# Optimization experiments

Hardware: AMD Instinct MI355X
Metric: run time of the kernel (lower is better)

Reference implementation:

```python
import jax, jax.numpy as jnp
import numpy as np

MAX_ITER = 10
EPS = 1e-4


def setup_inputs() -> dict:
    key = jax.random.key(0)
    k1, k2, k3 = jax.random.split(key, 3)
    B, N, M = 64, 1024, 1024
    s = jax.random.uniform(k1, (B, N, M), dtype=jnp.float32)
    nrows = jax.random.randint(k2, (B,), 0, N, dtype=jnp.int64 if jax.config.read('jax_enable_x64') else jnp.int32)
    ncols = jax.random.randint(k3, (B,), 0, M, dtype=nrows.dtype)
    return {"s": s, "nrows": nrows, "ncols": ncols}


def _sinkhorn(s, nrows, ncols):
    # Faithful to torch Sinkhorn.forward with exp=False, dummy_row=False.
    # The torch code builds [B,N,N]/[B,M,M] block-of-ones matrices and matmuls;
    # mathematically this is a masked column-sum (even iters) / row-sum (odd iters)
    # over the valid nrows[b] x ncols[b] block, followed by division inside the
    # block and zeroing outside it.
    B, N, M = s.shape
    row_mask = jnp.arange(N)[None, :] < nrows[:, None]            # [B, N]
    col_mask = jnp.arange(M)[None, :] < ncols[:, None]            # [B, M]
    mask = row_mask[:, :, None] & col_mask[:, None, :]            # [B, N, M]

    out = s + EPS
    for i in range(MAX_ITER):
        if i % 2 == 0:
            # column sums over valid rows -> [B, 1, M]
            sm = jnp.sum(jnp.where(row_mask[:, :, None], out, 0.0), axis=1, keepdims=True)
        else:
            # row sums over valid cols -> [B, N, 1]
            sm = jnp.sum(jnp.where(col_mask[:, None, :], out, 0.0), axis=2, keepdims=True)
        sm = jnp.where(sm == 0, 1.0, sm)  # guard (only affects masked-out entries)
        out = jnp.where(mask, out / sm, 0.0)
    return out


def reference(s, nrows, ncols):
    return _sinkhorn(s, nrows, ncols)
```

## Files before the change

kernel.cpp:

```cpp
#include <hip/hip_runtime.h>
#include <hip/hip_fp16.h>

#define EPS 1e-4f
constexpr int N_DIM = 1024;
constexpr int M_DIM = 1024;
constexpr int BATCH = 64;
constexpr int CH    = 16;
constexpr int CROWS = N_DIM / CH;



__global__ __launch_bounds__(256)
void col_first_conv(const float* __restrict__ s,
                    const int* __restrict__ nrows,
                    const int* __restrict__ ncols,
                    __half* __restrict__ h,
                    float* __restrict__ tpart) {
    const int b  = blockIdx.y;
    const int mt = blockIdx.x & 3;
    const int ch = blockIdx.x >> 2;
    const int R = nrows[b], C = ncols[b];
    const int lane = threadIdx.x & 63, wv = threadIdx.x >> 6;
    const int m = mt * 256 + lane * 4;
    const int n0 = ch * CROWS;
    const int nend = min(R, n0 + CROWS);
    const size_t base = (size_t)b * N_DIM * M_DIM;

    float4 acc = make_float4(0.f, 0.f, 0.f, 0.f);
    if (mt * 256 < C) {
        for (int n = n0 + wv; n < nend; n += 4) {
            float4 v = *(const float4*)(s + base + (size_t)n * M_DIM + m);
            v.x = (m + 0 < C) ? v.x + EPS : 0.f;
            v.y = (m + 1 < C) ? v.y + EPS : 0.f;
            v.z = (m + 2 < C) ? v.z + EPS : 0.f;
            v.w = (m + 3 < C) ? v.w + EPS : 0.f;
            acc.x += v.x; acc.y += v.y; acc.z += v.z; acc.w += v.w;
            union { __half2 h2[2]; uint2 u2; } pk;
            pk.h2[0] = __floats2half2_rn(v.x, v.y);
            pk.h2[1] = __floats2half2_rn(v.z, v.w);
            *(uint2*)(h + base + (size_t)n * M_DIM + m) = pk.u2;
        }
    } else {
        const uint2 z = make_uint2(0u, 0u);
        for (int n = n0 + wv; n < nend; n += 4)
            *(uint2*)(h + base + (size_t)n * M_DIM + m) = z;
    }
    __shared__ float4 red[4][64];
    red[wv][lane] = acc;
    __syncthreads();
    if (wv == 0) {
        float4 a0 = red[0][lane], a1 = red[1][lane],
               a2 = red[2][lane], a3 = red[3][lane];
        float4 t = make_float4(a0.x + a1.x + a2.x + a3.x,
                               a0.y + a1.y + a2.y + a3.y,
                               a0.z + a1.z + a2.z + a3.z,
                               a0.w + a1.w + a2.w + a3.w);
        *(float4*)(tpart + (size_t)(ch * BATCH + b) * M_DIM + m) = t;
    }
}

__global__ __launch_bounds__(256)
void col_h(const __half* __restrict__ h,
           const int* __restrict__ nrows,
           const int* __restrict__ ncols,
           const float* __restrict__ u,
           float* __restrict__ tpart) {
    const int b  = blockIdx.y;
    const int mt = blockIdx.x & 1;
    const int ch = blockIdx.x >> 1;
    const int R = nrows[b], C = ncols[b];
    const int lane = threadIdx.x & 63, wv = threadIdx.x >> 6;
    const int m = mt * 512 + lane * 8;
    const int n0 = ch * CROWS;
    const int nend = min(R, n0 + CROWS);
    const size_t base = (size_t)b * N_DIM * M_DIM;

    __shared__ float rlds[CROWS];
    if (threadIdx.x < CROWS) {
        float uu = u[b * N_DIM + n0 + threadIdx.x];
        rlds[threadIdx.x] = (uu == 0.f) ? 1.f : 1.f / uu;
    }
    __syncthreads();

    float acc[8] = {0.f, 0.f, 0.f, 0.f, 0.f, 0.f, 0.f, 0.f};
    if (mt * 512 < C) {
        for (int n = n0 + wv; n < nend; n += 4) {
            uint4 raw = *(const uint4*)(h + base + (size_t)n * M_DIM + m);
            const float rn = rlds[n - n0];
            const __half2* hp = (const __half2*)&raw;
#pragma unroll
            for (int k = 0; k < 4; ++k) {
                float2 f = __half22float2(hp[k]);
                acc[2 * k]     += rn * f.x;
                acc[2 * k + 1] += rn * f.y;
            }
        }
    }
    __shared__ float red[4][64 * 8];
#pragma unroll
    for (int k = 0; k < 8; ++k) red[wv][lane * 8 + k] = acc[k];
    __syncthreads();
    if (wv == 0) {
        float t[8];
#pragma unroll
        for (int k = 0; k < 8; ++k)
            t[k] = red[0][lane * 8 + k] + red[1][lane * 8 + k] +
                   red[2][lane * 8 + k] + red[3][lane * 8 + k];
        float* tp = tpart + (size_t)(ch * BATCH + b) * M_DIM + m;
        *(float4*)tp       = make_float4(t[0], t[1], t[2], t[3]);
        *(float4*)(tp + 4) = make_float4(t[4], t[5], t[6], t[7]);
    }
}

template <bool WRITE_C>
__global__ __launch_bounds__(256)
void row_h(const __half* __restrict__ h,
           const int* __restrict__ nrows,
           const int* __restrict__ ncols,
           const float* __restrict__ tpart,
           float* __restrict__ u,
           float* __restrict__ cOut) {
    const int b = blockIdx.y;
    const int R = nrows[b], C = ncols[b];
    const int n0 = blockIdx.x * 32;
    if (n0 >= R) return;
    const size_t base = (size_t)b * N_DIM * M_DIM;

    __shared__ float clds[M_DIM];
    {
        const int t4 = threadIdx.x * 4;
        float4 sum = make_float4(0.f, 0.f, 0.f, 0.f);
#pragma unroll
        for (int ch = 0; ch < CH; ++ch) {
            float4 p = *(const float4*)(tpart + (size_t)(ch * BATCH + b) * M_DIM + t4);
            sum.x += p.x; sum.y += p.y; sum.z += p.z; sum.w += p.w;
        }
        float4 cv;
        cv.x = (sum.x == 0.f) ? 1.f : 1.f / sum.x;
        cv.y = (sum.y == 0.f) ? 1.f : 1.f / sum.y;
        cv.z = (sum.z == 0.f) ? 1.f : 1.f / sum.z;
        cv.w = (sum.w == 0.f) ? 1.f : 1.f / sum.w;
        *(float4*)&clds[t4] = cv;
        if (WRITE_C && blockIdx.x == 0)
            *(float4*)(cOut + b * M_DIM + t4) = cv;
    }
    __syncthreads();

    const int lane = threadIdx.x & 63, wv = threadIdx.x >> 6;
    const bool hi = (C > 512);
#pragma unroll 2
    for (int i = 0; i < 8; ++i) {
        const int n = n0 + wv * 8 + i;
        if (n >= R) break;
        const __half* hrow = h + base + (size_t)n * M_DIM;
        float sum = 0.f;
        {
            uint4 raw = *(const uint4*)(hrow + lane * 8);
            const __half2* hp = (const __half2*)&raw;
            const float* cl = &clds[lane * 8];
#pragma unroll
            for (int k = 0; k < 4; ++k) {
                float2 f = __half22float2(hp[k]);
                sum += f.x * cl[2 * k] + f.y * cl[2 * k + 1];
            }
        }
        if (hi) {
            uint4 raw = *(const uint4*)(hrow + 512 + lane * 8);
            const __half2* hp = (const __half2*)&raw;
            const float* cl = &clds[512 + lane * 8];
#pragma unroll
            for (int k = 0; k < 4; ++k) {
                float2 f = __half22float2(hp[k]);
                sum += f.x * cl[2 * k] + f.y * cl[2 * k + 1];
            }
        }
#pragma unroll
        for (int off = 32; off; off >>= 1) sum += __shfl_down(sum, off);
        if (lane == 0) u[b * N_DIM + n] = sum;
    }
}

__global__ __launch_bounds__(256)
void finalize(const float* __restrict__ s,
              const int* __restrict__ nrows,
              const int* __restrict__ ncols,
              const float* __restrict__ u,
              const float* __restrict__ c,
              float* __restrict__ out) {
    const int n = blockIdx.x;
    const int b = blockIdx.y;
    const int R = nrows[b], C = ncols[b];
    const size_t base = ((size_t)b * N_DIM + n) * M_DIM;
    const int m = threadIdx.x * 4;

    float4 o = make_float4(0.f, 0.f, 0.f, 0.f);
    if (n < R && m < C) {
        float uu = u[b * N_DIM + n];
        float rn = (uu == 0.f) ? 1.f : 1.f / uu;
        float4 v  = *(const float4*)(s + base + m);
        float4 cc = *(const float4*)(c + b * M_DIM + m);
        o.x = (m + 0 < C) ? (v.x + EPS) * rn * cc.x : 0.f;
        o.y = (m + 1 < C) ? (v.y + EPS) * rn * cc.y : 0.f;
        o.z = (m + 2 < C) ? (v.z + EPS) * rn * cc.z : 0.f;
        o.w = (m + 3 < C) ? (v.w + EPS) * rn * cc.w : 0.f;
    }
    *(float4*)(out + base + m) = o;
}

template <bool FIRST, int CHUNKS>
__global__ __launch_bounds__(256)
void col_sweep(const float* __restrict__ s, const int* __restrict__ nrows,
               const int* __restrict__ ncols, const float* __restrict__ u,
               float* __restrict__ tpart) {
    const int b  = blockIdx.y;
    const int mt = blockIdx.x & 3;
    const int ch = blockIdx.x >> 2;
    const int R = nrows[b], C = ncols[b];
    const int lane = threadIdx.x & 63, wv = threadIdx.x >> 6;
    const int m0 = mt * 256;
    const int m  = m0 + lane * 4;
    constexpr int RW = N_DIM / CHUNKS;
    const int n0 = ch * RW;
    const int nend = min(R, n0 + RW);

    __shared__ float rlds[RW > 1024 ? 1 : RW];
    if (!FIRST) {
        for (int i = threadIdx.x; i < RW; i += 256) {
            float uu = u[b * N_DIM + n0 + i];
            rlds[i] = (uu == 0.f) ? 1.f : 1.f / uu;
        }
        __syncthreads();
    }
    float4 acc = make_float4(0.f, 0.f, 0.f, 0.f);
    if (m0 < C) {
        const float* __restrict__ sb = s + (size_t)b * N_DIM * M_DIM;
#pragma unroll 4
        for (int n = n0 + wv; n < nend; n += 4) {
            float4 v = *(const float4*)(sb + (size_t)n * M_DIM + m);
            float rn = FIRST ? 1.f : rlds[n - n0];
            acc.x += rn * (v.x + EPS); acc.y += rn * (v.y + EPS);
            acc.z += rn * (v.z + EPS); acc.w += rn * (v.w + EPS);
        }
    }
    __shared__ float4 red[4][64];
    red[wv][lane] = acc;
    __syncthreads();
    if (wv == 0) {
        float4 a0 = red[0][lane], a1 = red[1][lane],
               a2 = red[2][lane], a3 = red[3][lane];
        float4 t = make_float4(a0.x + a1.x + a2.x + a3.x, a0.y + a1.y + a2.y + a3.y,
                               a0.z + a1.z + a2.z + a3.z, a0.w + a1.w + a2.w + a3.w);
        *(float4*)(tpart + ((size_t)(ch * BATCH + b)) * M_DIM + m) = t;
    }
}

template <int CHUNKS, bool WRITE_C>
__global__ __launch_bounds__(256)
void row_sweep(const float* __restrict__ s, const int* __restrict__ nrows,
               const int* __restrict__ ncols, const float* __restrict__ tpart,
               float* __restrict__ u, float* __restrict__ cOut) {
    const int b = blockIdx.y;
    const int R = nrows[b], C = ncols[b];
    const int n0 = blockIdx.x * 16;
    if (n0 >= R) return;
    __shared__ float clds[M_DIM];
    {
        const int t4 = threadIdx.x;
        float4 sum = make_float4(0.f, 0.f, 0.f, 0.f);
#pragma unroll
        for (int ch = 0; ch < CHUNKS; ++ch) {
            float4 p = *(const float4*)(tpart + ((size_t)(ch * BATCH + b)) * M_DIM + t4 * 4);
            sum.x += p.x; sum.y += p.y; sum.z += p.z; sum.w += p.w;
        }
        float4 cv;
        cv.x = (sum.x == 0.f) ? 1.f : 1.f / sum.x;
        cv.y = (sum.y == 0.f) ? 1.f : 1.f / sum.y;
        cv.z = (sum.z == 0.f) ? 1.f : 1.f / sum.z;
        cv.w = (sum.w == 0.f) ? 1.f : 1.f / sum.w;
        *(float4*)&clds[t4 * 4] = cv;
        if (WRITE_C && blockIdx.x == 0)
            *(float4*)(cOut + b * M_DIM + t4 * 4) = cv;
    }
    __syncthreads();
    const int lane = threadIdx.x & 63, wv = threadIdx.x >> 6;
    const int C4 = C >> 2;
#pragma unroll
    for (int i = 0; i < 4; ++i) {
        const int n = n0 + wv * 4 + i;
        if (n >= R) break;
        const float* __restrict__ srow = s + ((size_t)b * N_DIM + n) * M_DIM;
        float sum = 0.f;
        for (int j = lane; j < C4; j += 64) {
            float4 v  = ((const float4*)srow)[j];
            float4 cc = *(const float4*)&clds[j * 4];
            sum += (v.x + EPS) * cc.x + (v.y + EPS) * cc.y +
                   (v.z + EPS) * cc.z + (v.w + EPS) * cc.w;
        }
        for (int mm = (C4 << 2) + lane; mm < C; mm += 64)
            sum += (srow[mm] + EPS) * clds[mm];
#pragma unroll
        for (int off = 32; off; off >>= 1) sum += __shfl_down(sum, off);
        if (lane == 0) u[b * N_DIM + n] = sum;
    }
}

extern "C" void kernel_launch(void* const* d_in, const int* in_sizes, int n_in,
                              void* d_out, int out_size, void* d_ws, size_t ws_size,
                              hipStream_t stream) {
    const float* s     = (const float*)d_in[0];
    const int*   nrows = (const int*)d_in[1];
    const int*   ncols = (const int*)d_in[2];
    float*       out   = (float*)d_out;

    const size_t hElems   = (size_t)BATCH * N_DIM * M_DIM;
    const size_t need_f16 = hElems * 2 +
                            ((size_t)CH * BATCH * M_DIM + BATCH * N_DIM + BATCH * M_DIM) * 4;

    if (ws_size >= need_f16) {
        __half* h     = (__half*)d_ws;
        float*  tpart = (float*)(h + hElems);
        float*  u     = tpart + (size_t)CH * BATCH * M_DIM;
        float*  c     = u + (size_t)BATCH * N_DIM;

        dim3 colGrid1(4 * CH, BATCH);
        dim3 colGridH(2 * CH, BATCH);
        dim3 rowGridH(32, BATCH);

        col_first_conv<<<colGrid1, 256, 0, stream>>>(s, nrows, ncols, h, tpart);
        row_h<false><<<rowGridH, 256, 0, stream>>>(h, nrows, ncols, tpart, u, c);
        for (int k = 0; k < 3; ++k) {
            col_h<<<colGridH, 256, 0, stream>>>(h, nrows, ncols, u, tpart);
            row_h<false><<<rowGridH, 256, 0, stream>>>(h, nrows, ncols, tpart, u, c);
        }
        col_h<<<colGridH, 256, 0, stream>>>(h, nrows, ncols, u, tpart);
        row_h<true><<<rowGridH, 256, 0, stream>>>(h, nrows, ncols, tpart, u, c);
        finalize<<<dim3(N_DIM, BATCH), 256, 0, stream>>>(s, nrows, ncols, u, c, out);
        return;
    }

    const size_t need4 = (size_t)(4 * BATCH * M_DIM + BATCH * N_DIM + BATCH * M_DIM) * 4;
    if (ws_size >= need4) {
        float* tpart = (float*)d_ws;
        float* u = tpart + (size_t)4 * BATCH * M_DIM;
        float* c = u + (size_t)BATCH * N_DIM;
        dim3 colGrid(16, BATCH), rowGrid(64, BATCH);
        col_sweep<true, 4><<<colGrid, 256, 0, stream>>>(s, nrows, ncols, u, tpart);
        row_sweep<4, false><<<rowGrid, 256, 0, stream>>>(s, nrows, ncols, tpart, u, c);
        for (int k = 1; k < 4; ++k) {
            col_sweep<false, 4><<<colGrid, 256, 0, stream>>>(s, nrows, ncols, u, tpart);
            row_sweep<4, false><<<rowGrid, 256, 0, stream>>>(s, nrows, ncols, tpart, u, c);
        }
        col_sweep<false, 4><<<colGrid, 256, 0, stream>>>(s, nrows, ncols, u, tpart);
        row_sweep<4, true><<<rowGrid, 256, 0, stream>>>(s, nrows, ncols, tpart, u, c);
        finalize<<<dim3(N_DIM, BATCH), 256, 0, stream>>>(s, nrows, ncols, u, c, out);
    } else {
        float* tpart = (float*)d_ws;
        float* u = tpart + (size_t)BATCH * M_DIM;
        float* c = u + (size_t)BATCH * N_DIM;
        dim3 colGrid(4, BATCH), rowGrid(64, BATCH);
        col_sweep<true, 1><<<colGrid, 256, 0, stream>>>(s, nrows, ncols, u, tpart);
        row_sweep<1, false><<<rowGrid, 256, 0, stream>>>(s, nrows, ncols, tpart, u, c);
        for (int k = 1; k < 4; ++k) {
            col_sweep<false, 1><<<colGrid, 256, 0, stream>>>(s, nrows, ncols, u, tpart);
            row_sweep<1, false><<<rowGrid, 256, 0, stream>>>(s, nrows, ncols, tpart, u, c);
        }
        col_sweep<false, 1><<<colGrid, 256, 0, stream>>>(s, nrows, ncols, u, tpart);
        row_sweep<1, true><<<rowGrid, 256, 0, stream>>>(s, nrows, ncols, tpart, u, c);
        finalize<<<dim3(N_DIM, BATCH), 256, 0, stream>>>(s, nrows, ncols, u, c, out);
    }
}
```

Baseline: 239.0 us.

## Fuse final row normalization with output write and halve column chunks

Replaces the last row_h plus finalize pass with a single row_final kernel that computes row sums from the fp16 copy, then immediately writes the normalized output from registers, avoiding a re-read of the fp32 input. Also reduces column-partial chunks from 16 to 8, fewer tpart partials to reduce at the cost of longer per-block row loops. The output is now derived from the fp16 copy rather than the original fp32 s, which may reduce accuracy.

```diff
diff --git a/kernel.cpp b/kernel.cpp
--- a/kernel.cpp
+++ b/kernel.cpp
@@ -5,7 +5,7 @@
 constexpr int N_DIM = 1024;
 constexpr int M_DIM = 1024;
 constexpr int BATCH = 64;
-constexpr int CH    = 16;
+constexpr int CH    = 8;
 constexpr int CROWS = N_DIM / CH;
 
 
@@ -76,9 +76,9 @@
     const size_t base = (size_t)b * N_DIM * M_DIM;
 
     __shared__ float rlds[CROWS];
-    if (threadIdx.x < CROWS) {
-        float uu = u[b * N_DIM + n0 + threadIdx.x];
-        rlds[threadIdx.x] = (uu == 0.f) ? 1.f : 1.f / uu;
+    for (int i = threadIdx.x; i < CROWS; i += 256) {
+        float uu = u[b * N_DIM + n0 + i];
+        rlds[i] = (uu == 0.f) ? 1.f : 1.f / uu;
     }
     __syncthreads();
 
@@ -112,14 +112,12 @@
     }
 }
 
-template <bool WRITE_C>
 __global__ __launch_bounds__(256)
 void row_h(const __half* __restrict__ h,
            const int* __restrict__ nrows,
            const int* __restrict__ ncols,
            const float* __restrict__ tpart,
-           float* __restrict__ u,
-           float* __restrict__ cOut) {
+           float* __restrict__ u) {
     const int b = blockIdx.y;
     const int R = nrows[b], C = ncols[b];
     const int n0 = blockIdx.x * 32;
@@ -141,8 +139,6 @@
         cv.z = (sum.z == 0.f) ? 1.f : 1.f / sum.z;
         cv.w = (sum.w == 0.f) ? 1.f : 1.f / sum.w;
         *(float4*)&clds[t4] = cv;
-        if (WRITE_C && blockIdx.x == 0)
-            *(float4*)(cOut + b * M_DIM + t4) = cv;
     }
     __syncthreads();
 
@@ -181,12 +177,194 @@
 }
 
 __global__ __launch_bounds__(256)
-void finalize(const float* __restrict__ s,
-              const int* __restrict__ nrows,
-              const int* __restrict__ ncols,
-              const float* __restrict__ u,
-              const float* __restrict__ c,
-              float* __restrict__ out) {
+void row_final(const __half* __restrict__ h,
+               const int* __restrict__ nrows,
+               const int* __restrict__ ncols,
+               const float* __restrict__ tpart,
+               float* __restrict__ out) {
+    const int b = blockIdx.y;
+    const int R = nrows[b], C = ncols[b];
+    const int n0 = blockIdx.x * 32;
+    const size_t base = (size_t)b * N_DIM * M_DIM;
+
+    __shared__ float clds[M_DIM];
+    {
+        const int t4 = threadIdx.x * 4;
+        float4 sum = make_float4(0.f, 0.f, 0.f, 0.f);
+#pragma unroll
+        for (int ch = 0; ch < CH; ++ch) {
+            float4 p = *(const float4*)(tpart + (size_t)(ch * BATCH + b) * M_DIM + t4);
+            sum.x += p.x; sum.y += p.y; sum.z += p.z; sum.w += p.w;
+        }
+        float4 cv;
+        cv.x = (sum.x == 0.f) ? 1.f : 1.f / sum.x;
+        cv.y = (sum.y == 0.f) ? 1.f : 1.f / sum.y;
+        cv.z = (sum.z == 0.f) ? 1.f : 1.f / sum.z;
+        cv.w = (sum.w == 0.f) ? 1.f : 1.f / sum.w;
+        *(float4*)&clds[t4] = cv;
+    }
+    __syncthreads();
+
+    const int lane = threadIdx.x & 63, wv = threadIdx.x >> 6;
+    const bool hi = (C > 512);
+    const float4 z4 = make_float4(0.f, 0.f, 0.f, 0.f);
+
+    for (int i = 0; i < 8; ++i) {
+        const int n = n0 + wv * 8 + i;
+        float* orow = out + base + (size_t)n * M_DIM;
+        float4 o0 = z4, o1 = z4, o2 = z4, o3 = z4;
+        if (n < R) {
+            const __half* hrow = h + base + (size_t)n * M_DIM;
+            uint4 rlo = *(const uint4*)(hrow + lane * 8);
+            uint4 rhi;
+            float flo[8], fhi[8];
+            const __half2* hp = (const __half2*)&rlo;
+#pragma unroll
+            for (int k = 0; k < 4; ++k) {
+                float2 f = __half22float2(hp[k]);
+                flo[2 * k] = f.x; flo[2 * k + 1] = f.y;
+            }
+            const float* cl = &clds[lane * 8];
+            float sum = 0.f;
+#pragma unroll
+            for (int k = 0; k < 8; ++k) sum += flo[k] * cl[k];
+            if (hi) {
+                rhi = *(const uint4*)(hrow + 512 + lane * 8);
+                const __half2* hq = (const __half2*)&rhi;
+#pragma unroll
+                for (int k = 0; k < 4; ++k) {
+                    float2 f = __half22float2(hq[k]);
+                    fhi[2 * k] = f.x; fhi[2 * k + 1] = f.y;
+                }
+                const float* ch2 = &clds[512 + lane * 8];
+#pragma unroll
+                for (int k = 0; k < 8; ++k) sum += fhi[k] * ch2[k];
+            }
+#pragma unroll
+            for (int off = 32; off; off >>= 1) sum += __shfl_down(sum, off);
+            float tot = __shfl(sum, 0);
+            const float rn = (tot == 0.f) ? 1.f : 1.f / tot;
+
+            o0 = make_float4(flo[0] * rn * cl[0], flo[1] * rn * cl[1],
+                             flo[2] * rn * cl[2], flo[3] * rn * cl[3]);
+            o1 = make_float4(flo[4] * rn * cl[4], flo[5] * rn * cl[5],
+                             flo[6] * rn * cl[6], flo[7] * rn * cl[7]);
+            if (hi) {
+                const float* ch2 = &clds[512 + lane * 8];
+                o2 = make_float4(fhi[0] * rn * ch2[0], fhi[1] * rn * ch2[1],
+                                 fhi[2] * rn * ch2[2], fhi[3] * rn * ch2[3]);
+                o3 = make_float4(fhi[4] * rn * ch2[4], fhi[5] * rn * ch2[5],
+                                 fhi[6] * rn * ch2[6], fhi[7] * rn * ch2[7]);
+            }
+        }
+        *(float4*)(orow + lane * 8)           = o0;
+        *(float4*)(orow + lane * 8 + 4)       = o1;
+        *(float4*)(orow + 512 + lane * 8)     = o2;
+        *(float4*)(orow + 512 + lane * 8 + 4) = o3;
+    }
+}
+
+template <bool FIRST, int CHUNKS>
+__global__ __launch_bounds__(256)
+void col_sweep(const float* __restrict__ s, const int* __restrict__ nrows,
+               const int* __restrict__ ncols, const float* __restrict__ u,
+               float* __restrict__ tpart) {
+    const int b  = blockIdx.y;
+    const int mt = blockIdx.x & 3;
+    const int ch = blockIdx.x >> 2;
+    const int R = nrows[b], C = ncols[b];
+    const int lane = threadIdx.x & 63, wv = threadIdx.x >> 6;
+    const int m0 = mt * 256;
+    const int m  = m0 + lane * 4;
+    constexpr int RW = N_DIM / CHUNKS;
+    const int n0 = ch * RW;
+    const int nend = min(R, n0 + RW);
+
+    __shared__ float rlds[RW > 1024 ? 1 : RW];
+    if (!FIRST) {
+        for (int i = threadIdx.x; i < RW; i += 256) {
+            float uu = u[b * N_DIM + n0 + i];
+            rlds[i] = (uu == 0.f) ? 1.f : 1.f / uu;
+        }
+        __syncthreads();
+    }
+    float4 acc = make_float4(0.f, 0.f, 0.f, 0.f);
+    if (m0 < C) {
+        const float* __restrict__ sb = s + (size_t)b * N_DIM * M_DIM;
+#pragma unroll 4
+        for (int n = n0 + wv; n < nend; n += 4) {
+            float4 v = *(const float4*)(sb + (size_t)n * M_DIM + m);
+            float rn = FIRST ? 1.f : rlds[n - n0];
+            acc.x += rn * (v.x + EPS); acc.y += rn * (v.y + EPS);
+            acc.z += rn * (v.z + EPS); acc.w += rn * (v.w + EPS);
+        }
+    }
+    __shared__ float4 red[4][64];
+    red[wv][lane] = acc;
+    __syncthreads();
+    if (wv == 0) {
+        float4 a0 = red[0][lane], a1 = red[1][lane],
+               a2 = red[2][lane], a3 = red[3][lane];
+        float4 t = make_float4(a0.x + a1.x + a2.x + a3.x, a0.y + a1.y + a2.y + a3.y,
+                               a0.z + a1.z + a2.z + a3.z, a0.w + a1.w + a2.w + a3.w);
+        *(float4*)(tpart + ((size_t)(ch * BATCH + b)) * M_DIM + m) = t;
+    }
+}
+
+template <int CHUNKS, bool WRITE_C>
+__global__ __launch_bounds__(256)
+void row_sweep(const float* __restrict__ s, const int* __restrict__ nrows,
+               const int* __restrict__ ncols, const float* __restrict__ tpart,
+               float* __restrict__ u, float* __restrict__ cOut) {
+    const int b = blockIdx.y;
+    const int R = nrows[b], C = ncols[b];
+    const int n0 = blockIdx.x * 16;
+    if (n0 >= R) return;
+    __shared__ float clds[M_DIM];
+    {
+        const int t4 = threadIdx.x;
+        float4 sum = make_float4(0.f, 0.f, 0.f, 0.f);
+#pragma unroll
+        for (int ch = 0; ch < CHUNKS; ++ch) {
+            float4 p = *(const float4*)(tpart + ((size_t)(ch * BATCH + b)) * M_DIM + t4 * 4);
+            sum.x += p.x; sum.y += p.y; sum.z += p.z; sum.w += p.w;
+        }
+        float4 cv;
+        cv.x = (sum.x == 0.f) ? 1.f : 1.f / sum.x;
+        cv.y = (sum.y == 0.f) ? 1.f : 1.f / sum.y;
+        cv.z = (sum.z == 0.f) ? 1.f : 1.f / sum.z;
+        cv.w = (sum.w == 0.f) ? 1.f : 1.f / sum.w;
+        *(float4*)&clds[t4 * 4] = cv;
+        if (WRITE_C && blockIdx.x == 0)
+            *(float4*)(cOut + b * M_DIM + t4 * 4) = cv;
+    }
+    __syncthreads();
+    const int lane = threadIdx.x & 63, wv = threadIdx.x >> 6;
+    const int C4 = C >> 2;
+#pragma unroll
+    for (int i = 0; i < 4; ++i) {
+        const int n = n0 + wv * 4 + i;
+        if (n >= R) break;
+        const float* __restrict__ srow = s + ((size_t)b * N_DIM + n) * M_DIM;
+        float sum = 0.f;
+        for (int j = lane; j < C4; j += 64) {
+            float4 v  = ((const float4*)srow)[j];
+            float4 cc = *(const float4*)&clds[j * 4];
+            sum += (v.x + EPS) * cc.x + (v.y + EPS) * cc.y +
+                   (v.z + EPS) * cc.z + (v.w + EPS) * cc.w;
+        }
+        for (int mm = (C4 << 2) + lane; mm < C; mm += 64)
+            sum += (srow[mm] + EPS) * clds[mm];
+#pragma unroll
+        for (int off = 32; off; off >>= 1) sum += __shfl_down(sum, off);
+        if (lane == 0) u[b * N_DIM + n] = sum;
+    }
+}
+
+__global__ __launch_bounds__(256)
+void finalize(const float* __restrict__ s, const int* __restrict__ nrows,
+              const int* __restrict__ ncols, const float* __restrict__ u,
+              const float* __restrict__ c, float* __restrict__ out) {
     const int n = blockIdx.x;
     const int b = blockIdx.y;
     const int R = nrows[b], C = ncols[b];
@@ -207,103 +385,6 @@
     *(float4*)(out + base + m) = o;
 }
 
-template <bool FIRST, int CHUNKS>
-__global__ __launch_bounds__(256)
-void col_sweep(const float* __restrict__ s, const int* __restrict__ nrows,
-               const int* __restrict__ ncols, const float* __restrict__ u,
-               float* __restrict__ tpart) {
-    const int b  = blockIdx.y;
-    const int mt = blockIdx.x & 3;
-    const int ch = blockIdx.x >> 2;
-    const int R = nrows[b], C = ncols[b];
-    const int lane = threadIdx.x & 63, wv = threadIdx.x >> 6;
-    const int m0 = mt * 256;
-    const int m  = m0 + lane * 4;
-    constexpr int RW = N_DIM / CHUNKS;
-    const int n0 = ch * RW;
-    const int nend = min(R, n0 + RW);
-
-    __shared__ float rlds[RW > 1024 ? 1 : RW];
-    if (!FIRST) {
-        for (int i = threadIdx.x; i < RW; i += 256) {
-            float uu = u[b * N_DIM + n0 + i];
-            rlds[i] = (uu == 0.f) ? 1.f : 1.f / uu;
-        }
-        __syncthreads();
-    }
-    float4 acc = make_float4(0.f, 0.f, 0.f, 0.f);
-    if (m0 < C) {
-        const float* __restrict__ sb = s + (size_t)b * N_DIM * M_DIM;
-#pragma unroll 4
-        for (int n = n0 + wv; n < nend; n += 4) {
-            float4 v = *(const float4*)(sb + (size_t)n * M_DIM + m);
-            float rn = FIRST ? 1.f : rlds[n - n0];
-            acc.x += rn * (v.x + EPS); acc.y += rn * (v.y + EPS);
-            acc.z += rn * (v.z + EPS); acc.w += rn * (v.w + EPS);
-        }
-    }
-    __shared__ float4 red[4][64];
-    red[wv][lane] = acc;
-    __syncthreads();
-    if (wv == 0) {
-        float4 a0 = red[0][lane], a1 = red[1][lane],
-               a2 = red[2][lane], a3 = red[3][lane];
-        float4 t = make_float4(a0.x + a1.x + a2.x + a3.x, a0.y + a1.y + a2.y + a3.y,
-                               a0.z + a1.z + a2.z + a3.z, a0.w + a1.w + a2.w + a3.w);
-        *(float4*)(tpart + ((size_t)(ch * BATCH + b)) * M_DIM + m) = t;
-    }
-}
-
-template <int CHUNKS, bool WRITE_C>
-__global__ __launch_bounds__(256)
-void row_sweep(const float* __restrict__ s, const int* __restrict__ nrows,
-               const int* __restrict__ ncols, const float* __restrict__ tpart,
-               float* __restrict__ u, float* __restrict__ cOut) {
-    const int b = blockIdx.y;
-    const int R = nrows[b], C = ncols[b];
-    const int n0 = blockIdx.x * 16;
-    if (n0 >= R) return;
-    __shared__ float clds[M_DIM];
-    {
-        const int t4 = threadIdx.x;
-        float4 sum = make_float4(0.f, 0.f, 0.f, 0.f);
-#pragma unroll
-        for (int ch = 0; ch < CHUNKS; ++ch) {
-            float4 p = *(const float4*)(tpart + ((size_t)(ch * BATCH + b)) * M_DIM + t4 * 4);
-            sum.x += p.x; sum.y += p.y; sum.z += p.z; sum.w += p.w;
-        }
-        float4 cv;
-        cv.x = (sum.x == 0.f) ? 1.f : 1.f / sum.x;
-        cv.y = (sum.y == 0.f) ? 1.f : 1.f / sum.y;
-        cv.z = (sum.z == 0.f) ? 1.f : 1.f / sum.z;
-        cv.w = (sum.w == 0.f) ? 1.f : 1.f / sum.w;
-        *(float4*)&clds[t4 * 4] = cv;
-        if (WRITE_C && blockIdx.x == 0)
-            *(float4*)(cOut + b * M_DIM + t4 * 4) = cv;
-    }
-    __syncthreads();
-    const int lane = threadIdx.x & 63, wv = threadIdx.x >> 6;
-    const int C4 = C >> 2;
-#pragma unroll
-    for (int i = 0; i < 4; ++i) {
-        const int n = n0 + wv * 4 + i;
-        if (n >= R) break;
-        const float* __restrict__ srow = s + ((size_t)b * N_DIM + n) * M_DIM;
-        float sum = 0.f;
-        for (int j = lane; j < C4; j += 64) {
-            float4 v  = ((const float4*)srow)[j];
-            float4 cc = *(const float4*)&clds[j * 4];
-            sum += (v.x + EPS) * cc.x + (v.y + EPS) * cc.y +
-                   (v.z + EPS) * cc.z + (v.w + EPS) * cc.w;
-        }
-        for (int mm = (C4 << 2) + lane; mm < C; mm += 64)
-            sum += (srow[mm] + EPS) * clds[mm];
-#pragma unroll
-        for (int off = 32; off; off >>= 1) sum += __shfl_down(sum, off);
-        if (lane == 0) u[b * N_DIM + n] = sum;
-    }
-}
-
 extern "C" void kernel_launch(void* const* d_in, const int* in_sizes, int n_in,
                               void* d_out, int out_size, void* d_ws, size_t ws_size,
                               hipStream_t stream) {
@@ -314,27 +395,25 @@
 
     const size_t hElems   = (size_t)BATCH * N_DIM * M_DIM;
     const size_t need_f16 = hElems * 2 +
-                            ((size_t)CH * BATCH * M_DIM + BATCH * N_DIM + BATCH * M_DIM) * 4;
+                            ((size_t)CH * BATCH * M_DIM + BATCH * N_DIM) * 4;
 
     if (ws_size >= need_f16) {
         __half* h     = (__half*)d_ws;
         float*  tpart = (float*)(h + hElems);
         float*  u     = tpart + (size_t)CH * BATCH * M_DIM;
-        float*  c     = u + (size_t)BATCH * N_DIM;
 
         dim3 colGrid1(4 * CH, BATCH);
         dim3 colGridH(2 * CH, BATCH);
         dim3 rowGridH(32, BATCH);
 
         col_first_conv<<<colGrid1, 256, 0, stream>>>(s, nrows, ncols, h, tpart);
-        row_h<false><<<rowGridH, 256, 0, stream>>>(h, nrows, ncols, tpart, u, c);
+        row_h<<<rowGridH, 256, 0, stream>>>(h, nrows, ncols, tpart, u);
         for (int k = 0; k < 3; ++k) {
             col_h<<<colGridH, 256, 0, stream>>>(h, nrows, ncols, u, tpart);
-            row_h<false><<<rowGridH, 256, 0, stream>>>(h, nrows, ncols, tpart, u, c);
+            row_h<<<rowGridH, 256, 0, stream>>>(h, nrows, ncols, tpart, u);
         }
         col_h<<<colGridH, 256, 0, stream>>>(h, nrows, ncols, u, tpart);
-        row_h<true><<<rowGridH, 256, 0, stream>>>(h, nrows, ncols, tpart, u, c);
-        finalize<<<dim3(N_DIM, BATCH), 256, 0, stream>>>(s, nrows, ncols, u, c, out);
+        row_final<<<rowGridH, 256, 0, stream>>>(h, nrows, ncols, tpart, out);
         return;
     }
 
```

Result: no change. 235.0 us (-1.7%).

## Fuse row and column sweeps into single fp16 pass per iteration

Applied to the files above, without the earlier changes.

Each Sinkhorn row-normalisation step now computes row sums over the fp16 copy and, in the same pass, accumulates the next column partial sums, using ping-pong partial buffers. The last step writes the final output directly, so the separate column kernels and the finalize kernel that reread the fp32 input are gone. Each iteration now reads the half matrix once instead of twice, and launch count drops. Grid parallelism per kernel shrinks to 16 blocks per batch, which may under-occupy the device, and the output is now derived from fp16 values instead of the original fp32 input.

```diff
diff --git a/kernel.cpp b/kernel.cpp
--- a/kernel.cpp
+++ b/kernel.cpp
@@ -9,20 +9,20 @@
 constexpr int CROWS = N_DIM / CH;
 
 
-
-__global__ __launch_bounds__(256)
-void col_first_conv(const float* __restrict__ s,
-                    const int* __restrict__ nrows,
-                    const int* __restrict__ ncols,
-                    __half* __restrict__ h,
-                    float* __restrict__ tpart) {
+__global__ __launch_bounds__(256)
+void conv_col0(const float* __restrict__ s,
+               const int* __restrict__ nrows,
+               const int* __restrict__ ncols,
+               __half* __restrict__ h,
+               float* __restrict__ tp0) {
     const int b  = blockIdx.y;
     const int mt = blockIdx.x & 3;
     const int ch = blockIdx.x >> 2;
     const int R = nrows[b], C = ncols[b];
+    const int n0 = ch * CROWS;
+    if (n0 >= R) return;
     const int lane = threadIdx.x & 63, wv = threadIdx.x >> 6;
     const int m = mt * 256 + lane * 4;
-    const int n0 = ch * CROWS;
     const int nend = min(R, n0 + CROWS);
     const size_t base = (size_t)b * N_DIM * M_DIM;
 
@@ -55,84 +55,218 @@
                                a0.y + a1.y + a2.y + a3.y,
                                a0.z + a1.z + a2.z + a3.z,
                                a0.w + a1.w + a2.w + a3.w);
-        *(float4*)(tpart + (size_t)(ch * BATCH + b) * M_DIM + m) = t;
-    }
-}
-
-__global__ __launch_bounds__(256)
-void col_h(const __half* __restrict__ h,
-           const int* __restrict__ nrows,
-           const int* __restrict__ ncols,
-           const float* __restrict__ u,
-           float* __restrict__ tpart) {
+        *(float4*)(tp0 + (size_t)(ch * BATCH + b) * M_DIM + m) = t;
+    }
+}
+
+template <bool FINAL>
+__global__ __launch_bounds__(256)
+void row_step(const __half* __restrict__ h,
+              const int* __restrict__ nrows,
+              const int* __restrict__ ncols,
+              const float* __restrict__ tpIn,
+              float* __restrict__ tpOut,
+              float* __restrict__ out) {
     const int b  = blockIdx.y;
-    const int mt = blockIdx.x & 1;
-    const int ch = blockIdx.x >> 1;
-    const int R = nrows[b], C = ncols[b];
+    const int ch = blockIdx.x;
+    const int R = nrows[b], C = ncols[b];
+    const int n0 = ch * CROWS;
+    if (!FINAL && n0 >= R) return;
     const int lane = threadIdx.x & 63, wv = threadIdx.x >> 6;
-    const int m = mt * 512 + lane * 8;
-    const int n0 = ch * CROWS;
-    const int nend = min(R, n0 + CROWS);
     const size_t base = (size_t)b * N_DIM * M_DIM;
-
-    __shared__ float rlds[CROWS];
-    if (threadIdx.x < CROWS) {
-        float uu = u[b * N_DIM + n0 + threadIdx.x];
-        rlds[threadIdx.x] = (uu == 0.f) ? 1.f : 1.f / uu;
-    }
-    __syncthreads();
-
-    float acc[8] = {0.f, 0.f, 0.f, 0.f, 0.f, 0.f, 0.f, 0.f};
-    if (mt * 512 < C) {
+    const bool hi = (C > 512);
+    const bool anyrows = (n0 < R);
+
+    __shared__ float clds[M_DIM];
+    __shared__ float tp_lds[4][M_DIM];
+
+    float crlo[8], crhi[8];
+    if (anyrows) {
+        const int nch = min(CH, (R + CROWS - 1) / CROWS);
+        const int t4 = threadIdx.x * 4;
+        if (hi || t4 < 512) {
+            float4 sum = make_float4(0.f, 0.f, 0.f, 0.f);
+            for (int cc = 0; cc < nch; ++cc) {
+                float4 p = *(const float4*)(tpIn + (size_t)(cc * BATCH + b) * M_DIM + t4);
+                sum.x += p.x; sum.y += p.y; sum.z += p.z; sum.w += p.w;
+            }
+            float4 cv;
+            cv.x = (sum.x == 0.f) ? 1.f : 1.f / sum.x;
+            cv.y = (sum.y == 0.f) ? 1.f : 1.f / sum.y;
+            cv.z = (sum.z == 0.f) ? 1.f : 1.f / sum.z;
+            cv.w = (sum.w == 0.f) ? 1.f : 1.f / sum.w;
+            *(float4*)&clds[t4] = cv;
+        }
+        __syncthreads();
+        {
+            float4 a = *(const float4*)&clds[lane * 8];
+            float4 bb = *(const float4*)&clds[lane * 8 + 4];
+            crlo[0]=a.x; crlo[1]=a.y; crlo[2]=a.z; crlo[3]=a.w;
+            crlo[4]=bb.x; crlo[5]=bb.y; crlo[6]=bb.z; crlo[7]=bb.w;
+            if (hi) {
+                float4 d = *(const float4*)&clds[512 + lane * 8];
+                float4 e = *(const float4*)&clds[512 + lane * 8 + 4];
+                crhi[0]=d.x; crhi[1]=d.y; crhi[2]=d.z; crhi[3]=d.w;
+                crhi[4]=e.x; crhi[5]=e.y; crhi[6]=e.z; crhi[7]=e.w;
+            }
+        }
+    }
+
+    float tplo[8] = {0,0,0,0,0,0,0,0};
+    float tphi[8] = {0,0,0,0,0,0,0,0};
+
+    for (int i = 0; i < 16; ++i) {
+        const int n = n0 + wv * 16 + i;
+        if (n < R) {
+            const __half* hrow = h + base + (size_t)n * M_DIM;
+            uint4 rlo = *(const uint4*)(hrow + lane * 8);
+            float flo[8];
+            {
+                const __half2* hp = (const __half2*)&rlo;
+#pragma unroll
+                for (int k = 0; k < 4; ++k) {
+                    float2 f = __half22float2(hp[k]);
+                    flo[2*k] = f.x; flo[2*k+1] = f.y;
+                }
+            }
+            float dot = 0.f;
+#pragma unroll
+            for (int k = 0; k < 8; ++k) dot += flo[k] * crlo[k];
+            float fhi[8];
+            if (hi) {
+                uint4 rhi = *(const uint4*)(hrow + 512 + lane * 8);
+                const __half2* hq = (const __half2*)&rhi;
+#pragma unroll
+                for (int k = 0; k < 4; ++k) {
+                    float2 f = __half22float2(hq[k]);
+                    fhi[2*k] = f.x; fhi[2*k+1] = f.y;
+                }
+#pragma unroll
+                for (int k = 0; k < 8; ++k) dot += fhi[k] * crhi[k];
+            }
+#pragma unroll
+            for (int off = 32; off; off >>= 1) dot += __shfl_xor(dot, off);
+            const float r = (dot == 0.f) ? 1.f : 1.f / dot;
+
+            if (FINAL) {
+                float* orow = out + base + (size_t)n * M_DIM;
+                float4 o0 = make_float4(flo[0]*r*crlo[0], flo[1]*r*crlo[1],
+                                        flo[2]*r*crlo[2], flo[3]*r*crlo[3]);
+                float4 o1 = make_float4(flo[4]*r*crlo[4], flo[5]*r*crlo[5],
+                                        flo[6]*r*crlo[6], flo[7]*r*crlo[7]);
+                *(float4*)(orow + lane * 8)     = o0;
+                *(float4*)(orow + lane * 8 + 4) = o1;
+                float4 o2 = make_float4(0.f,0.f,0.f,0.f), o3 = o2;
+                if (hi) {
+                    o2 = make_float4(fhi[0]*r*crhi[0], fhi[1]*r*crhi[1],
+                                     fhi[2]*r*crhi[2], fhi[3]*r*crhi[3]);
+                    o3 = make_float4(fhi[4]*r*crhi[4], fhi[5]*r*crhi[5],
+                                     fhi[6]*r*crhi[6], fhi[7]*r*crhi[7]);
+                }
+                *(float4*)(orow + 512 + lane * 8)     = o2;
+                *(float4*)(orow + 512 + lane * 8 + 4) = o3;
+            } else {
+#pragma unroll
+                for (int k = 0; k < 8; ++k) tplo[k] += flo[k] * r;
+                if (hi) {
+#pragma unroll
+                    for (int k = 0; k < 8; ++k) tphi[k] += fhi[k] * r;
+                }
+            }
+        } else if (FINAL) {
+            float* orow = out + base + (size_t)n * M_DIM;
+            const float4 z = make_float4(0.f, 0.f, 0.f, 0.f);
+            *(float4*)(orow + lane * 8)           = z;
+            *(float4*)(orow + lane * 8 + 4)       = z;
+            *(float4*)(orow + 512 + lane * 8)     = z;
+            *(float4*)(orow + 512 + lane * 8 + 4) = z;
+        }
+    }
+
+    if (!FINAL) {
+#pragma unroll
+        for (int k = 0; k < 8; ++k) tp_lds[wv][lane * 8 + k] = tplo[k];
+        if (hi) {
+#pragma unroll
+            for (int k = 0; k < 8; ++k) tp_lds[wv][512 + lane * 8 + k] = tphi[k];
+        }
+        __syncthreads();
+        const int t4 = threadIdx.x * 4;
+        if (hi || t4 < 512) {
+            float4 s0 = *(const float4*)&tp_lds[0][t4];
+            float4 s1 = *(const float4*)&tp_lds[1][t4];
+            float4 s2 = *(const float4*)&tp_lds[2][t4];
+            float4 s3 = *(const float4*)&tp_lds[3][t4];
+            float4 t = make_float4(s0.x+s1.x+s2.x+s3.x, s0.y+s1.y+s2.y+s3.y,
+                                   s0.z+s1.z+s2.z+s3.z, s0.w+s1.w+s2.w+s3.w);
+            *(float4*)(tpOut + (size_t)(ch * BATCH + b) * M_DIM + t4) = t;
+        }
+    }
+}
+
+template <bool FIRST, int CHUNKS>
+__global__ __launch_bounds__(256)
+void col_sweep(const float* __restrict__ s, const int* __restrict__ nrows,
+               const int* __restrict__ ncols, const float* __restrict__ u,
+               float* __restrict__ tpart) {
+    const int b  = blockIdx.y;
+    const int mt = blockIdx.x & 3;
+    const int ch = blockIdx.x >> 2;
+    const int R = nrows[b], C = ncols[b];
+    const int lane = threadIdx.x & 63, wv = threadIdx.x >> 6;
+    const int m0 = mt * 256;
+    const int m  = m0 + lane * 4;
+    constexpr int RW = N_DIM / CHUNKS;
+    const int n0 = ch * RW;
+    const int nend = min(R, n0 + RW);
+
+    __shared__ float rlds[RW > 1024 ? 1 : RW];
+    if (!FIRST) {
+        for (int i = threadIdx.x; i < RW; i += 256) {
+            float uu = u[b * N_DIM + n0 + i];
+            rlds[i] = (uu == 0.f) ? 1.f : 1.f / uu;
+        }
+        __syncthreads();
+    }
+    float4 acc = make_float4(0.f, 0.f, 0.f, 0.f);
+    if (m0 < C) {
+        const float* __restrict__ sb = s + (size_t)b * N_DIM * M_DIM;
+#pragma unroll 4
         for (int n = n0 + wv; n < nend; n += 4) {
-            uint4 raw = *(const uint4*)(h + base + (size_t)n * M_DIM + m);
-            const float rn = rlds[n - n0];
-            const __half2* hp = (const __half2*)&raw;
-#pragma unroll
-            for (int k = 0; k < 4; ++k) {
-                float2 f = __half22float2(hp[k]);
-                acc[2 * k]     += rn * f.x;
-                acc[2 * k + 1] += rn * f.y;
-            }
-        }
-    }
-    __shared__ float red[4][64 * 8];
-#pragma unroll
-    for (int k = 0; k < 8; ++k) red[wv][lane * 8 + k] = acc[k];
+            float4 v = *(const float4*)(sb + (size_t)n * M_DIM + m);
+            float rn = FIRST ? 1.f : rlds[n - n0];
+            acc.x += rn * (v.x + EPS); acc.y += rn * (v.y + EPS);
+            acc.z += rn * (v.z + EPS); acc.w += rn * (v.w + EPS);
+        }
+    }
+    __shared__ float4 red[4][64];
+    red[wv][lane] = acc;
     __syncthreads();
     if (wv == 0) {
-        float t[8];
-#pragma unroll
-        for (int k = 0; k < 8; ++k)
-            t[k] = red[0][lane * 8 + k] + red[1][lane * 8 + k] +
-                   red[2][lane * 8 + k] + red[3][lane * 8 + k];
-        float* tp = tpart + (size_t)(ch * BATCH + b) * M_DIM + m;
-        *(float4*)tp       = make_float4(t[0], t[1], t[2], t[3]);
-        *(float4*)(tp + 4) = make_float4(t[4], t[5], t[6], t[7]);
-    }
-}
-
-template <bool WRITE_C>
-__global__ __launch_bounds__(256)
-void row_h(const __half* __restrict__ h,
-           const int* __restrict__ nrows,
-           const int* __restrict__ ncols,
-           const float* __restrict__ tpart,
-           float* __restrict__ u,
-           float* __restrict__ cOut) {
+        float4 a0 = red[0][lane], a1 = red[1][lane],
+               a2 = red[2][lane], a3 = red[3][lane];
+        float4 t = make_float4(a0.x + a1.x + a2.x + a3.x, a0.y + a1.y + a2.y + a3.y,
+                               a0.z + a1.z + a2.z + a3.z, a0.w + a1.w + a2.w + a3.w);
+        *(float4*)(tpart + ((size_t)(ch * BATCH + b)) * M_DIM + m) = t;
+    }
+}
+
+template <int CHUNKS, bool WRITE_C>
+__global__ __launch_bounds__(256)
+void row_sweep(const float* __restrict__ s, const int* __restrict__ nrows,
+               const int* __restrict__ ncols, const float* __restrict__ tpart,
+               float* __restrict__ u, float* __restrict__ cOut) {
     const int b = blockIdx.y;
     const int R = nrows[b], C = ncols[b];
-    const int n0 = blockIdx.x * 32;
+    const int n0 = blockIdx.x * 16;
     if (n0 >= R) return;
-    const size_t base = (size_t)b * N_DIM * M_DIM;
-
     __shared__ float clds[M_DIM];
     {
-        const int t4 = threadIdx.x * 4;
+        const int t4 = threadIdx.x;
         float4 sum = make_float4(0.f, 0.f, 0.f, 0.f);
 #pragma unroll
-        for (int ch = 0; ch < CH; ++ch) {
-            float4 p = *(const float4*)(tpart + (size_t)(ch * BATCH + b) * M_DIM + t4);
+        for (int ch = 0; ch < CHUNKS; ++ch) {
+            float4 p = *(const float4*)(tpart + ((size_t)(ch * BATCH + b)) * M_DIM + t4 * 4);
             sum.x += p.x; sum.y += p.y; sum.z += p.z; sum.w += p.w;
         }
         float4 cv;
@@ -140,40 +274,27 @@
         cv.y = (sum.y == 0.f) ? 1.f : 1.f / sum.y;
         cv.z = (sum.z == 0.f) ? 1.f : 1.f / sum.z;
         cv.w = (sum.w == 0.f) ? 1.f : 1.f / sum.w;
-        *(float4*)&clds[t4] = cv;
+        *(float4*)&clds[t4 * 4] = cv;
         if (WRITE_C && blockIdx.x == 0)
-            *(float4*)(cOut + b * M_DIM + t4) = cv;
+            *(float4*)(cOut + b * M_DIM + t4 * 4) = cv;
     }
     __syncthreads();
-
     const int lane = threadIdx.x & 63, wv = threadIdx.x >> 6;
-    const bool hi = (C > 512);
-#pragma unroll 2
-    for (int i = 0; i < 8; ++i) {
-        const int n = n0 + wv * 8 + i;
+    const int C4 = C >> 2;
+#pragma unroll
+    for (int i = 0; i < 4; ++i) {
+        const int n = n0 + wv * 4 + i;
         if (n >= R) break;
-        const __half* hrow = h + base + (size_t)n * M_DIM;
+        const float* __restrict__ srow = s + ((size_t)b * N_DIM + n) * M_DIM;
         float sum = 0.f;
-        {
-            uint4 raw = *(const uint4*)(hrow + lane * 8);
-            const __half2* hp = (const __half2*)&raw;
-            const float* cl = &clds[lane * 8];
-#pragma unroll
-            for (int k = 0; k < 4; ++k) {
-                float2 f = __half22float2(hp[k]);
-                sum += f.x * cl[2 * k] + f.y * cl[2 * k + 1];
-            }
-        }
-        if (hi) {
-            uint4 raw = *(const uint4*)(hrow + 512 + lane * 8);
-            const __half2* hp = (const __half2*)&raw;
-            const float* cl = &clds[512 + lane * 8];
-#pragma unroll
-            for (int k = 0; k < 4; ++k) {
-                float2 f = __half22float2(hp[k]);
-                sum += f.x * cl[2 * k] + f.y * cl[2 * k + 1];
-            }
-        }
+        for (int j = lane; j < C4; j += 64) {
+            float4 v  = ((const float4*)srow)[j];
+            float4 cc = *(const float4*)&clds[j * 4];
+            sum += (v.x + EPS) * cc.x + (v.y + EPS) * cc.y +
+                   (v.z + EPS) * cc.z + (v.w + EPS) * cc.w;
+        }
+        for (int mm = (C4 << 2) + lane; mm < C; mm += 64)
+            sum += (srow[mm] + EPS) * clds[mm];
 #pragma unroll
         for (int off = 32; off; off >>= 1) sum += __shfl_down(sum, off);
         if (lane == 0) u[b * N_DIM + n] = sum;
@@ -181,12 +302,9 @@
 }
 
 __global__ __launch_bounds__(256)
-void finalize(const float* __restrict__ s,
-              const int* __restrict__ nrows,
-              const int* __restrict__ ncols,
-              const float* __restrict__ u,
-              const float* __restrict__ c,
-              float* __restrict__ out) {
+void finalize(const float* __restrict__ s, const int* __restrict__ nrows,
+              const int* __restrict__ ncols, const float* __restrict__ u,
+              const float* __restrict__ c, float* __restrict__ out) {
     const int n = blockIdx.x;
     const int b = blockIdx.y;
     const int R = nrows[b], C = ncols[b];
@@ -207,103 +325,6 @@
     *(float4*)(out + base + m) = o;
 }
 
-template <bool FIRST, int CHUNKS>
-__global__ __launch_bounds__(256)
-void col_sweep(const float* __restrict__ s, const int* __restrict__ nrows,
-               const int* __restrict__ ncols, const float* __restrict__ u,
-               float* __restrict__ tpart) {
-    const int b  = blockIdx.y;
-    const int mt = blockIdx.x & 3;
-    const int ch = blockIdx.x >> 2;
-    const int R = nrows[b], C = ncols[b];
-    const int lane = threadIdx.x & 63, wv = threadIdx.x >> 6;
-    const int m0 = mt * 256;
-    const int m  = m0 + lane * 4;
-    constexpr int RW = N_DIM / CHUNKS;
-    const int n0 = ch * RW;
-    const int nend = min(R, n0 + RW);
-
-    __shared__ float rlds[RW > 1024 ? 1 : RW];
-    if (!FIRST) {
-        for (int i = threadIdx.x; i < RW; i += 256) {
-            float uu = u[b * N_DIM + n0 + i];
-            rlds[i] = (uu == 0.f) ? 1.f : 1.f / uu;
-        }
-        __syncthreads();
-    }
-    float4 acc = make_float4(0.f, 0.f, 0.f, 0.f);
-    if (m0 < C) {
-        const float* __restrict__ sb = s + (size_t)b * N_DIM * M_DIM;
-#pragma unroll 4
-        for (int n = n0 + wv; n < nend; n += 4) {
-            float4 v = *(const float4*)(sb + (size_t)n * M_DIM + m);
-            float rn = FIRST ? 1.f : rlds[n - n0];
-            acc.x += rn * (v.x + EPS); acc.y += rn * (v.y + EPS);
-            acc.z += rn * (v.z + EPS); acc.w += rn * (v.w + EPS);
-        }
-    }
-    __shared__ float4 red[4][64];
-    red[wv][lane] = acc;
-    __syncthreads();
-    if (wv == 0) {
-        float4 a0 = red[0][lane], a1 = red[1][lane],
-               a2 = red[2][lane], a3 = red[3][lane];
-        float4 t = make_float4(a0.x + a1.x + a2.x + a3.x, a0.y + a1.y + a2.y + a3.y,
-                               a0.z + a1.z + a2.z + a3.z, a0.w + a1.w + a2.w + a3.w);
-        *(float4*)(tpart + ((size_t)(ch * BATCH + b)) * M_DIM + m) = t;
-    }
-}
-
-template <int CHUNKS, bool WRITE_C>
-__global__ __launch_bounds__(256)
-void row_sweep(const float* __restrict__ s, const int* __restrict__ nrows,
-               const int* __restrict__ ncols, const float* __restrict__ tpart,
-               float* __restrict__ u, float* __restrict__ cOut) {
-    const int b = blockIdx.y;
-    const int R = nrows[b], C = ncols[b];
-    const int n0 = blockIdx.x * 16;
-    if (n0 >= R) return;
-    __shared__ float clds[M_DIM];
-    {
-        const int t4 = threadIdx.x;
-        float4 sum = make_float4(0.f, 0.f, 0.f, 0.f);
-#pragma unroll
-        for (int ch = 0; ch < CHUNKS; ++ch) {
-            float4 p = *(const float4*)(tpart + ((size_t)(ch * BATCH + b)) * M_DIM + t4 * 4);
-            sum.x += p.x; sum.y += p.y; sum.z += p.z; sum.w += p.w;
-        }
-        float4 cv;
-        cv.x = (sum.x == 0.f) ? 1.f : 1.f / sum.x;
-        cv.y = (sum.y == 0.f) ? 1.f : 1.f / sum.y;
-        cv.z = (sum.z == 0.f) ? 1.f : 1.f / sum.z;
-        cv.w = (sum.w == 0.f) ? 1.f : 1.f / sum.w;
-        *(float4*)&clds[t4 * 4] = cv;
-        if (WRITE_C && blockIdx.x == 0)
-            *(float4*)(cOut + b * M_DIM + t4 * 4) = cv;
-    }
-    __syncthreads();
-    const int lane = threadIdx.x & 63, wv = threadIdx.x >> 6;
-    const int C4 = C >> 2;
-#pragma unroll
-    for (int i = 0; i < 4; ++i) {
-        const int n = n0 + wv * 4 + i;
-        if (n >= R) break;
-        const float* __restrict__ srow = s + ((size_t)b * N_DIM + n) * M_DIM;
-        float sum = 0.f;
-        for (int j = lane; j < C4; j += 64) {
-            float4 v  = ((const float4*)srow)[j];
-            float4 cc = *(const float4*)&clds[j * 4];
-            sum += (v.x + EPS) * cc.x + (v.y + EPS) * cc.y +
-                   (v.z + EPS) * cc.z + (v.w + EPS) * cc.w;
-        }
-        for (int mm = (C4 << 2) + lane; mm < C; mm += 64)
-            sum += (srow[mm] + EPS) * clds[mm];
-#pragma unroll
-        for (int off = 32; off; off >>= 1) sum += __shfl_down(sum, off);
-        if (lane == 0) u[b * N_DIM + n] = sum;
-    }
-}
-
 extern "C" void kernel_launch(void* const* d_in, const int* in_sizes, int n_in,
                               void* d_out, int out_size, void* d_ws, size_t ws_size,
                               hipStream_t stream) {
@@ -313,34 +334,29 @@
     float*       out   = (float*)d_out;
 
     const size_t hElems   = (size_t)BATCH * N_DIM * M_DIM;
-    const size_t need_f16 = hElems * 2 +
-                            ((size_t)CH * BATCH * M_DIM + BATCH * N_DIM + BATCH * M_DIM) * 4;
+    const size_t tpElems  = (size_t)CH * BATCH * M_DIM;
+    const size_t need_f16 = hElems * 2 + 2 * tpElems * 4;
 
     if (ws_size >= need_f16) {
-        __half* h     = (__half*)d_ws;
-        float*  tpart = (float*)(h + hElems);
-        float*  u     = tpart + (size_t)CH * BATCH * M_DIM;
-        float*  c     = u + (size_t)BATCH * N_DIM;
-
-        dim3 colGrid1(4 * CH, BATCH);
-        dim3 colGridH(2 * CH, BATCH);
-        dim3 rowGridH(32, BATCH);
-
-        col_first_conv<<<colGrid1, 256, 0, stream>>>(s, nrows, ncols, h, tpart);
-        row_h<false><<<rowGridH, 256, 0, stream>>>(h, nrows, ncols, tpart, u, c);
-        for (int k = 0; k < 3; ++k) {
-            col_h<<<colGridH, 256, 0, stream>>>(h, nrows, ncols, u, tpart);
-            row_h<false><<<rowGridH, 256, 0, stream>>>(h, nrows, ncols, tpart, u, c);
-        }
-        col_h<<<colGridH, 256, 0, stream>>>(h, nrows, ncols, u, tpart);
-        row_h<true><<<rowGridH, 256, 0, stream>>>(h, nrows, ncols, tpart, u, c);
-        finalize<<<dim3(N_DIM, BATCH), 256, 0, stream>>>(s, nrows, ncols, u, c, out);
+        __half* h   = (__half*)d_ws;
+        float*  tp0 = (float*)(h + hElems);
+        float*  tp1 = tp0 + tpElems;
+
+        dim3 convGrid(4 * CH, BATCH);
+        dim3 kGrid(CH, BATCH);
+
+        conv_col0<<<convGrid, 256, 0, stream>>>(s, nrows, ncols, h, tp0);
+        row_step<false><<<kGrid, 256, 0, stream>>>(h, nrows, ncols, tp0, tp1, out);
+        row_step<false><<<kGrid, 256, 0, stream>>>(h, nrows, ncols, tp1, tp0, out);
+        row_step<false><<<kGrid, 256, 0, stream>>>(h, nrows, ncols, tp0, tp1, out);
+        row_step<false><<<kGrid, 256, 0, stream>>>(h, nrows, ncols, tp1, tp0, out);
+        row_step<true ><<<kGrid, 256, 0, stream>>>(h, nrows, ncols, tp0, tp1, out);
         return;
     }
 
     const size_t need4 = (size_t)(4 * BATCH * M_DIM + BATCH * N_DIM + BATCH * M_DIM) * 4;
+    float* tpart = (float*)d_ws;
     if (ws_size >= need4) {
-        float* tpart = (float*)d_ws;
         float* u = tpart + (size_t)4 * BATCH * M_DIM;
         float* c = u + (size_t)BATCH * N_DIM;
         dim3 colGrid(16, BATCH), rowGrid(64, BATCH);
@@ -354,7 +370,6 @@
         row_sweep<4, true><<<rowGrid, 256, 0, stream>>>(s, nrows, ncols, tpart, u, c);
         finalize<<<dim3(N_DIM, BATCH), 256, 0, stream>>>(s, nrows, ncols, u, c, out);
     } else {
-        float* tpart = (float*)d_ws;
         float* u = tpart + (size_t)BATCH * M_DIM;
         float* c = u + (size_t)BATCH * N_DIM;
         dim3 colGrid(4, BATCH), rowGrid(64, BATCH);
```

Measured after the change: 210.4 us. -12.0%, faster.
